# Performance work log

Hardware: AMD Instinct MI355X
Metric: run time of the kernel (lower is better)

Reference implementation:

```python
import jax, jax.numpy as jnp
import numpy as np

DIM = 512
HEADS = 8
BLOCK = 64
EXPAND = 4
EPS = 1e-5


def _layernorm(x, g, b):
    m = jnp.mean(x, axis=-1, keepdims=True)
    v = jnp.mean((x - m) ** 2, axis=-1, keepdims=True)
    return (x - m) * jax.lax.rsqrt(v + EPS) * g + b


def setup_inputs() -> dict:
    key = jax.random.key(0)
    ks = jax.random.split(key, 8)
    B, L = 8, 4096
    x = jax.random.normal(ks[0], (B, DIM, L), dtype=jnp.float32)
    s = 0.02
    params = {
        'w_qkv': jax.random.normal(ks[1], (DIM, 3 * DIM), jnp.float32) * s,
        'b_qkv': jnp.zeros((3 * DIM,), jnp.float32),
        'w_proj': jax.random.normal(ks[2], (DIM, DIM), jnp.float32) * s,
        'b_proj': jnp.zeros((DIM,), jnp.float32),
        'ln1_g': jnp.ones((DIM,), jnp.float32),
        'ln1_b': jnp.zeros((DIM,), jnp.float32),
        'ln2_g': jnp.ones((DIM,), jnp.float32),
        'ln2_b': jnp.zeros((DIM,), jnp.float32),
        'w_ffn1': jax.random.normal(ks[3], (DIM, DIM * EXPAND), jnp.float32) * s,
        'b_ffn1': jnp.zeros((DIM * EXPAND,), jnp.float32),
        'w_ffn2': jax.random.normal(ks[4], (DIM * EXPAND // 2, DIM), jnp.float32) * s,
        'b_ffn2': jnp.zeros((DIM,), jnp.float32),
        'attn_scale': jnp.ones((DIM,), jnp.float32),
        'attn_bias': jnp.zeros((DIM,), jnp.float32),
        'mlp_scale': jnp.ones((DIM,), jnp.float32),
        'mlp_bias': jnp.zeros((DIM,), jnp.float32),
    }
    return {'x': x, **params}


def _block_attn(x, w_qkv, b_qkv, w_proj, b_proj):
    # x: (B, L, D); L % BLOCK == 0 (no padding branch)
    B, L, D = x.shape
    d = D // HEADS
    scale = d ** -0.5
    qkv = x @ w_qkv + b_qkv                       # (B, L, 3D)
    qkv = qkv.reshape(B, L, HEADS, 3 * d)         # per-head [q|k|v] layout (matches torch split)
    q, k, v = jnp.split(qkv, 3, axis=-1)          # each (B, L, H, d)
    nb = L // BLOCK
    def to_blocks(t):
        return t.transpose(0, 2, 1, 3).reshape(B, HEADS, nb, BLOCK, d)
    q, k, v = to_blocks(q), to_blocks(k), to_blocks(v)
    attn = jnp.einsum('bhnqd,bhnkd->bhnqk', q, k) * scale
    attn = jax.nn.softmax(attn, axis=-1)
    o = jnp.einsum('bhnqk,bhnkd->bhnqd', attn, v)  # (B,H,nb,BLOCK,d)
    o = o.reshape(B, HEADS, L, d).transpose(0, 2, 1, 3).reshape(B, L, D)
    return o @ w_proj + b_proj


def _glu_mlp(x, w1, b1, w2, b2):
    h = x @ w1 + b1
    out, gate = jnp.split(h, 2, axis=-1)
    h = out * jax.nn.silu(gate)
    return h @ w2 + b2


def reference(x, w_qkv, b_qkv, w_proj, b_proj, ln1_g, ln1_b, ln2_g, ln2_b,
              w_ffn1, b_ffn1, w_ffn2, b_ffn2, attn_scale, attn_bias,
              mlp_scale, mlp_bias):
    # x: (B, DIM, L) channel-first, transposed inside like the torch module
    xt = x.transpose(0, 2, 1)                      # (B, L, D)
    # post-norm (prenorm=False)
    a = _block_attn(xt, w_qkv, b_qkv, w_proj, b_proj)
    a = a * attn_scale + attn_bias
    h = _layernorm(a + xt, ln1_g, ln1_b)
    m = _glu_mlp(h, w_ffn1, b_ffn1, w_ffn2, b_ffn2)
    m = m * mlp_scale + mlp_bias
    out = _layernorm(m + h, ln2_g, ln2_b)
    return out.transpose(0, 2, 1)                  # back to (B, DIM, L)
```

## Files before the change

### kernel.cpp

```cpp
#include <hip/hip_runtime.h>

#define DIM   512
#define LSEQ  4096
#define BATCH 8
#define NTOK  (BATCH * LSEQ)
#define NCHUNK 4
#define MCH   (NTOK / NCHUNK)
#define FCH   (NTOK / 2)

typedef __bf16 bf16_t;
typedef bf16_t bf16x8 __attribute__((ext_vector_type(8)));
typedef float  f32x4  __attribute__((ext_vector_type(4)));

__device__ __forceinline__ unsigned short f2bf(float f) {
  unsigned u = __builtin_bit_cast(unsigned, f);
  unsigned r = u + 0x7fffu + ((u >> 16) & 1u);
  return (unsigned short)(r >> 16);
}
__device__ __forceinline__ float bf2f(unsigned short s) {
  return __builtin_bit_cast(float, ((unsigned)s) << 16);
}
__device__ __forceinline__ bf16x8 ld_frag(const unsigned short* p) {
  uint4 v = *reinterpret_cast<const uint4*>(p);
  return __builtin_bit_cast(bf16x8, v);
}
__device__ __forceinline__ void gload16(const unsigned short* g, unsigned short* l) {
  __builtin_amdgcn_global_load_lds(
      (const __attribute__((address_space(1))) unsigned int*)(const void*)g,
      (__attribute__((address_space(3))) unsigned int*)(void*)l, 16, 0, 0);
}

__global__ __launch_bounds__(256) void prep_w(
    const float* __restrict__ W, unsigned short* __restrict__ out,
    int N, int NB, int ffn1) {
  const int idx = blockIdx.x * 256 + threadIdx.x;
  const int j0 = (idx & 7) * 8;
  const int nn = (idx >> 3) & 127;
  const int nbkt = idx >> 10;
  const int nb = nbkt % NB;
  const int kt = nbkt / NB;
  int wcol;
  if (ffn1) {
    int isg = (nn >> 5) & 1;
    int gcol = ((nn >> 6) << 5) + (((nn >> 4) & 1) << 4) + (nn & 15);
    wcol = isg * 1024 + nb * 64 + gcol;
  } else {
    wcol = nb * 128 + nn;
  }
  const int s = (nn & 7) << 3;
  union { unsigned short us[8]; uint4 u; } r;
#pragma unroll
  for (int t = 0; t < 8; ++t) {
    int row = kt * 64 + ((j0 ^ s) + t);
    r.us[t] = f2bf(W[(size_t)row * N + wcol]);
  }
  *reinterpret_cast<uint4*>(out + (size_t)nbkt * 8192 + nn * 64 + j0) = r.u;
}

__global__ __launch_bounds__(256) void transpose_in(
    const float* __restrict__ in, unsigned short* __restrict__ out) {
  __shared__ float tile[64][65];
  const int b = blockIdx.z;
  const int r0 = blockIdx.y * 64, c0 = blockIdx.x * 64;
  const float* ip = in + ((size_t)b * 512 + r0) * 4096 + c0;
#pragma unroll
  for (int i = 0; i < 16; ++i) {
    int flat = i * 256 + threadIdx.x;
    int r = flat >> 6, c = flat & 63;
    tile[r][c] = ip[(size_t)r * 4096 + c];
  }
  __syncthreads();
#pragma unroll
  for (int i = 0; i < 16; ++i) {
    int flat = i * 256 + threadIdx.x;
    int r = flat >> 6, c = flat & 63;
    out[((size_t)b * 4096 + c0 + r) * 512 + r0 + c] = f2bf(tile[c][r]);
  }
}

template <bool SCALERES>
__global__ __launch_bounds__(256, 2) void gemm_kernel(
    const unsigned short* __restrict__ A, const unsigned short* __restrict__ Wt,
    const float* __restrict__ bias, const float* __restrict__ scale,
    const float* __restrict__ bias2, const unsigned short* __restrict__ res,
    unsigned short* __restrict__ Cout, int N, int K, int nxb) {
  __shared__ unsigned short As[128 * 64];
  __shared__ unsigned short Bs[256 * 64];
  const int tid = threadIdx.x, lane = tid & 63, wave = tid >> 6;
  const int l15 = lane & 15, hi8 = (lane >> 4) * 8;
  const int wm = wave >> 1, wn = wave & 1;
  const int cpx = gridDim.x >> 3;
  const int sid = (blockIdx.x & 7) * cpx + (blockIdx.x >> 3);
  const int by = sid / nxb, bx = sid - by * nxb;
  const int row0 = by * 128, col0 = bx * 256;

  const unsigned short* abase =
      A + (size_t)(row0 + (lane >> 3)) * K + 8 * ((lane & 7) ^ (lane >> 3));
  const unsigned short* bbase = Wt + (size_t)(2 * bx) * 8192 + lane * 8;
  const size_t bstride = (size_t)(N >> 7) * 8192;

  f32x4 acc[4][8] = {};

  for (int kt = 0; kt < K; kt += 64) {
#pragma unroll
    for (int c = 0; c < 4; ++c) {
      const int ch = wave * 4 + c;
      gload16(abase + (size_t)(ch * 8) * K + kt, &As[ch * 512]);
    }
#pragma unroll
    for (int c = 0; c < 8; ++c) {
      const int cb = wave * 8 + c;
      gload16(bbase + (size_t)(kt >> 6) * bstride + cb * 512, &Bs[cb * 512]);
    }
    __syncthreads();
#pragma unroll
    for (int kk = 0; kk < 2; ++kk) {
      const int kbs = kk * 32 + hi8;
      bf16x8 af[4], bfr[8];
#pragma unroll
      for (int m = 0; m < 4; ++m) {
        int r = wm * 64 + m * 16 + l15;
        af[m] = ld_frag(&As[r * 64 + (kbs ^ ((r & 7) << 3))]);
      }
#pragma unroll
      for (int n = 0; n < 8; ++n) {
        int rb = wn * 128 + n * 16 + l15;
        bfr[n] = ld_frag(&Bs[rb * 64 + (kbs ^ ((rb & 7) << 3))]);
      }
#pragma unroll
      for (int m = 0; m < 4; ++m)
#pragma unroll
        for (int n = 0; n < 8; ++n)
          acc[m][n] = __builtin_amdgcn_mfma_f32_16x16x32_bf16(
              af[m], bfr[n], acc[m][n], 0, 0, 0);
    }
    __syncthreads();
  }
#pragma unroll
  for (int m = 0; m < 4; ++m) {
#pragma unroll
    for (int n = 0; n < 8; ++n) {
      const int col = col0 + wn * 128 + n * 16 + l15;
      const float b1 = bias[col];
      float sc = 1.f, b2 = 0.f;
      if constexpr (SCALERES) { sc = scale[col]; b2 = bias2[col]; }
#pragma unroll
      for (int r = 0; r < 4; ++r) {
        const int row = row0 + wm * 64 + m * 16 + (lane >> 4) * 4 + r;
        float v = acc[m][n][r] + b1;
        if constexpr (SCALERES) {
          v = v * sc + b2;
          v += bf2f(res[(size_t)row * N + col]);
        }
        Cout[(size_t)row * N + col] = f2bf(v);
      }
    }
  }
}

__global__ __launch_bounds__(256, 2) void ffn1glu_kernel(
    const unsigned short* __restrict__ A, const unsigned short* __restrict__ Wt,
    const float* __restrict__ b1, unsigned short* __restrict__ g, int nxb) {
  __shared__ unsigned short As[128 * 64];
  __shared__ unsigned short Bs[256 * 64];
  const int tid = threadIdx.x, lane = tid & 63, wave = tid >> 6;
  const int l15 = lane & 15, hi8 = (lane >> 4) * 8;
  const int wm = wave >> 1, wn = wave & 1;
  const int cpx = gridDim.x >> 3;
  const int sid = (blockIdx.x & 7) * cpx + (blockIdx.x >> 3);
  const int by = sid / nxb, bx = sid - by * nxb;
  const int row0 = by * 128;
  const int K = 512;

  const unsigned short* abase =
      A + (size_t)(row0 + (lane >> 3)) * K + 8 * ((lane & 7) ^ (lane >> 3));
  const unsigned short* bbase = Wt + (size_t)(2 * bx) * 8192 + lane * 8;
  const size_t bstride = (size_t)16 * 8192;

  f32x4 acc[4][8] = {};

  for (int kt = 0; kt < K; kt += 64) {
#pragma unroll
    for (int c = 0; c < 4; ++c) {
      const int ch = wave * 4 + c;
      gload16(abase + (size_t)(ch * 8) * K + kt, &As[ch * 512]);
    }
#pragma unroll
    for (int c = 0; c < 8; ++c) {
      const int cb = wave * 8 + c;
      gload16(bbase + (size_t)(kt >> 6) * bstride + cb * 512, &Bs[cb * 512]);
    }
    __syncthreads();
#pragma unroll
    for (int kk = 0; kk < 2; ++kk) {
      const int kbs = kk * 32 + hi8;
      bf16x8 af[4], bfr[8];
#pragma unroll
      for (int m = 0; m < 4; ++m) {
        int r = wm * 64 + m * 16 + l15;
        af[m] = ld_frag(&As[r * 64 + (kbs ^ ((r & 7) << 3))]);
      }
#pragma unroll
      for (int n = 0; n < 8; ++n) {
        int rb = wn * 128 + n * 16 + l15;
        bfr[n] = ld_frag(&Bs[rb * 64 + (kbs ^ ((rb & 7) << 3))]);
      }
#pragma unroll
      for (int m = 0; m < 4; ++m)
#pragma unroll
        for (int n = 0; n < 8; ++n)
          acc[m][n] = __builtin_amdgcn_mfma_f32_16x16x32_bf16(
              af[m], bfr[n], acc[m][n], 0, 0, 0);
    }
    __syncthreads();
  }
#pragma unroll
  for (int m = 0; m < 4; ++m) {
#pragma unroll
    for (int np = 0; np < 4; ++np) {
      const int n = (np & 1) + (np >> 1) * 4;
      const int sub = ((n & 4) ? 32 : 0) + (n & 1) * 16 + l15;
      const int gc = (2 * bx + wn) * 64 + sub;
      const float bo = b1[gc];
      const float bg = b1[1024 + gc];
#pragma unroll
      for (int r = 0; r < 4; ++r) {
        const int row = row0 + wm * 64 + m * 16 + (lane >> 4) * 4 + r;
        float o  = acc[m][n][r] + bo;
        float ga = acc[m][n + 2][r] + bg;
        float s  = ga / (1.f + __expf(-ga));
        g[(size_t)row * 1024 + gc] = f2bf(o * s);
      }
    }
  }
}

__global__ __launch_bounds__(256) void attn_kernel(
    const unsigned short* __restrict__ qkv, unsigned short* __restrict__ out) {
  __shared__ unsigned short Qs[64 * 64];
  __shared__ unsigned short Ks[64 * 64];
  __shared__ unsigned short Vs[64 * 64];
  __shared__ unsigned short Ps[64 * 64];
  const int id = blockIdx.x;
  const int h = id & 7, blk = id >> 3;
  const size_t tok0 = (size_t)blk * 64;
  const unsigned short* base = qkv + tok0 * 1536 + h * 192;
  const int tid = threadIdx.x, lane = tid & 63, wave = tid >> 6;

#pragma unroll
  for (int i = 0; i < 2; ++i) {
    int flat = i * 2048 + tid * 8;
    int r = flat >> 6, c = flat & 63;
    const unsigned short* p = base + (size_t)r * 1536 + c;
    uint4 q8 = *reinterpret_cast<const uint4*>(p);
    uint4 k8 = *reinterpret_cast<const uint4*>(p + 64);
    uint4 v8 = *reinterpret_cast<const uint4*>(p + 128);
    int us = r * 64 + (c ^ ((r & 7) << 3));
    *reinterpret_cast<uint4*>(&Qs[us]) = q8;
    *reinterpret_cast<uint4*>(&Ks[us]) = k8;
    const unsigned short* ve = reinterpret_cast<const unsigned short*>(&v8);
#pragma unroll
    for (int j = 0; j < 8; ++j) {
      int d = c + j;
      Vs[d * 64 + (r ^ ((d & 7) << 3))] = ve[j];
    }
  }
  __syncthreads();

  f32x4 sacc[4] = {};
#pragma unroll
  for (int kk = 0; kk < 64; kk += 32) {
    const int kb = kk + (lane >> 4) * 8;
    const int rq = wave * 16 + (lane & 15);
    bf16x8 aq = ld_frag(&Qs[rq * 64 + (kb ^ ((rq & 7) << 3))]);
#pragma unroll
    for (int n = 0; n < 4; ++n) {
      const int rk = n * 16 + (lane & 15);
      bf16x8 bk = ld_frag(&Ks[rk * 64 + (kb ^ ((rk & 7) << 3))]);
      sacc[n] = __builtin_amdgcn_mfma_f32_16x16x32_bf16(aq, bk, sacc[n], 0, 0, 0);
    }
  }
#pragma unroll
  for (int r = 0; r < 4; ++r) {
    float mx = -1e30f;
#pragma unroll
    for (int n = 0; n < 4; ++n) mx = fmaxf(mx, sacc[n][r]);
#pragma unroll
    for (int msk = 1; msk < 16; msk <<= 1) mx = fmaxf(mx, __shfl_xor(mx, msk));
    float sum = 0.f;
#pragma unroll
    for (int n = 0; n < 4; ++n) {
      float e = __expf((sacc[n][r] - mx) * 0.125f);
      sacc[n][r] = e;
      sum += e;
    }
#pragma unroll
    for (int msk = 1; msk < 16; msk <<= 1) sum += __shfl_xor(sum, msk);
    const float inv = 1.f / sum;
    const int row = wave * 16 + (lane >> 4) * 4 + r;
#pragma unroll
    for (int n = 0; n < 4; ++n) {
      int col = n * 16 + (lane & 15);
      Ps[row * 64 + (col ^ ((row & 7) << 3))] = f2bf(sacc[n][r] * inv);
    }
  }
  __syncthreads();

  f32x4 oacc[4] = {};
#pragma unroll
  for (int kk = 0; kk < 64; kk += 32) {
    const int kb = kk + (lane >> 4) * 8;
    const int rp = wave * 16 + (lane & 15);
    bf16x8 ap = ld_frag(&Ps[rp * 64 + (kb ^ ((rp & 7) << 3))]);
#pragma unroll
    for (int n = 0; n < 4; ++n) {
      const int rv = n * 16 + (lane & 15);
      bf16x8 bv = ld_frag(&Vs[rv * 64 + (kb ^ ((rv & 7) << 3))]);
      oacc[n] = __builtin_amdgcn_mfma_f32_16x16x32_bf16(ap, bv, oacc[n], 0, 0, 0);
    }
  }
#pragma unroll
  for (int n = 0; n < 4; ++n) {
    const int col = n * 16 + (lane & 15);
#pragma unroll
    for (int r = 0; r < 4; ++r) {
      const int row = wave * 16 + (lane >> 4) * 4 + r;
      out[(tok0 + row) * 512 + h * 64 + col] = f2bf(oacc[n][r]);
    }
  }
}

__global__ __launch_bounds__(256) void ln_kernel(
    const unsigned short* __restrict__ in, const float* __restrict__ gam,
    const float* __restrict__ bet, unsigned short* __restrict__ out) {
  const int wave = threadIdx.x >> 6, lane = threadIdx.x & 63;
  const size_t tok = (size_t)blockIdx.x * 4 + wave;
  const unsigned short* p = in + tok * DIM + lane * 8;
  uint4 raw = *reinterpret_cast<const uint4*>(p);
  const unsigned short* us = reinterpret_cast<const unsigned short*>(&raw);
  float x[8];
#pragma unroll
  for (int j = 0; j < 8; ++j) x[j] = bf2f(us[j]);
  float s = 0.f;
#pragma unroll
  for (int j = 0; j < 8; ++j) s += x[j];
#pragma unroll
  for (int m = 1; m < 64; m <<= 1) s += __shfl_xor(s, m);
  const float mean = s * (1.f / 512.f);
  float vr = 0.f;
#pragma unroll
  for (int j = 0; j < 8; ++j) { x[j] -= mean; vr += x[j] * x[j]; }
#pragma unroll
  for (int m = 1; m < 64; m <<= 1) vr += __shfl_xor(vr, m);
  const float rs = rsqrtf(vr * (1.f / 512.f) + 1e-5f);
  alignas(16) float gv[8], bv[8];
  *reinterpret_cast<float4*>(&gv[0]) = *reinterpret_cast<const float4*>(gam + lane * 8);
  *reinterpret_cast<float4*>(&gv[4]) = *reinterpret_cast<const float4*>(gam + lane * 8 + 4);
  *reinterpret_cast<float4*>(&bv[0]) = *reinterpret_cast<const float4*>(bet + lane * 8);
  *reinterpret_cast<float4*>(&bv[4]) = *reinterpret_cast<const float4*>(bet + lane * 8 + 4);
  union { unsigned short us[8]; uint4 u; } rr;
#pragma unroll
  for (int j = 0; j < 8; ++j) rr.us[j] = f2bf(x[j] * rs * gv[j] + bv[j]);
  unsigned short* q = out + tok * DIM + lane * 8;
  *reinterpret_cast<uint4*>(q) = rr.u;
}

__global__ __launch_bounds__(256) void ln_stats(
    const unsigned short* __restrict__ in, float2* __restrict__ stats) {
  const int wave = threadIdx.x >> 6, lane = threadIdx.x & 63;
  const size_t tok = (size_t)blockIdx.x * 4 + wave;
  const unsigned short* p = in + tok * DIM + lane * 8;
  uint4 raw = *reinterpret_cast<const uint4*>(p);
  const unsigned short* us = reinterpret_cast<const unsigned short*>(&raw);
  float x[8], s = 0.f;
#pragma unroll
  for (int j = 0; j < 8; ++j) { x[j] = bf2f(us[j]); s += x[j]; }
#pragma unroll
  for (int m = 1; m < 64; m <<= 1) s += __shfl_xor(s, m);
  const float mean = s * (1.f / 512.f);
  float vr = 0.f;
#pragma unroll
  for (int j = 0; j < 8; ++j) { float d = x[j] - mean; vr += d * d; }
#pragma unroll
  for (int m = 1; m < 64; m <<= 1) vr += __shfl_xor(vr, m);
  if (lane == 0) stats[tok] = make_float2(mean, rsqrtf(vr * (1.f / 512.f) + 1e-5f));
}

__global__ __launch_bounds__(256) void transpose_norm(
    const unsigned short* __restrict__ in, const float2* __restrict__ stats,
    const float* __restrict__ gam, const float* __restrict__ bet,
    float* __restrict__ out, int batch0) {
  __shared__ float tile[64][65];
  const int bz = blockIdx.z;
  const int b = batch0 + bz;
  const int t0 = blockIdx.y * 64, d0 = blockIdx.x * 64;
#pragma unroll
  for (int i = 0; i < 2; ++i) {
    int flat = i * 256 + threadIdx.x;
    int r = flat >> 3, cg = flat & 7;
    const size_t tokL = (size_t)bz * 4096 + t0 + r;
    uint4 raw = *reinterpret_cast<const uint4*>(in + tokL * 512 + d0 + cg * 8);
    const unsigned short* us = reinterpret_cast<const unsigned short*>(&raw);
    const float2 st = stats[tokL];
    alignas(16) float gv[8], bv[8];
    *reinterpret_cast<float4*>(&gv[0]) = *reinterpret_cast<const float4*>(gam + d0 + cg * 8);
    *reinterpret_cast<float4*>(&gv[4]) = *reinterpret_cast<const float4*>(gam + d0 + cg * 8 + 4);
    *reinterpret_cast<float4*>(&bv[0]) = *reinterpret_cast<const float4*>(bet + d0 + cg * 8);
    *reinterpret_cast<float4*>(&bv[4]) = *reinterpret_cast<const float4*>(bet + d0 + cg * 8 + 4);
#pragma unroll
    for (int j = 0; j < 8; ++j)
      tile[r][cg * 8 + j] = (bf2f(us[j]) - st.x) * st.y * gv[j] + bv[j];
  }
  __syncthreads();
#pragma unroll
  for (int i = 0; i < 16; ++i) {
    int flat = i * 256 + threadIdx.x;
    int r = flat >> 6, c = flat & 63;
    out[((size_t)b * 512 + d0 + r) * 4096 + t0 + c] = tile[c][r];
  }
}

extern "C" void kernel_launch(void* const* d_in, const int* in_sizes, int n_in,
                              void* d_out, int out_size, void* d_ws, size_t ws_size,
                              hipStream_t stream) {
  const float* x          = (const float*)d_in[0];
  const float* w_qkv      = (const float*)d_in[1];
  const float* b_qkv      = (const float*)d_in[2];
  const float* w_proj     = (const float*)d_in[3];
  const float* b_proj     = (const float*)d_in[4];
  const float* ln1_g      = (const float*)d_in[5];
  const float* ln1_b      = (const float*)d_in[6];
  const float* ln2_g      = (const float*)d_in[7];
  const float* ln2_b      = (const float*)d_in[8];
  const float* w_ffn1     = (const float*)d_in[9];
  const float* b_ffn1     = (const float*)d_in[10];
  const float* w_ffn2     = (const float*)d_in[11];
  const float* b_ffn2     = (const float*)d_in[12];
  const float* attn_scale = (const float*)d_in[13];
  const float* attn_bias  = (const float*)d_in[14];
  const float* mlp_scale  = (const float*)d_in[15];
  const float* mlp_bias   = (const float*)d_in[16];

  char* ws = (char*)d_ws;
  const size_t MiB = 1024ull * 1024ull;
  unsigned short* wqkvT  = (unsigned short*)(ws + 0);
  unsigned short* wprojT = (unsigned short*)(ws + 3 * MiB / 2);
  unsigned short* wffn1T = (unsigned short*)(ws + 2 * MiB);
  unsigned short* wffn2T = (unsigned short*)(ws + 4 * MiB);
  unsigned short* xt     = (unsigned short*)(ws + 5 * MiB);
  unsigned short* qkvH   = (unsigned short*)(ws + 37 * MiB);
  unsigned short* gbufC  = (unsigned short*)(ws + 5 * MiB);
  unsigned short* mresC  = (unsigned short*)(ws + 37 * MiB);
  float2*         st2    = (float2*)(ws + 53 * MiB);
  unsigned short* ares  = (unsigned short*)d_out;
  unsigned short* attnO = (unsigned short*)d_out + (size_t)NTOK * 512;
  unsigned short* hbuf  = (unsigned short*)d_out + (size_t)NTOK * 512;

  dim3 B256(256);
  prep_w<<<dim3(384), B256, 0, stream>>>(w_qkv,  wqkvT,  1536, 12, 0);
  prep_w<<<dim3(128), B256, 0, stream>>>(w_proj, wprojT,  512,  4, 0);
  prep_w<<<dim3(512), B256, 0, stream>>>(w_ffn1, wffn1T, 2048, 16, 1);
  prep_w<<<dim3(256), B256, 0, stream>>>(w_ffn2, wffn2T,  512,  4, 0);
  transpose_in<<<dim3(64, 8, 8), B256, 0, stream>>>(x, xt);
  for (int c = 0; c < NCHUNK; ++c) {
    gemm_kernel<false><<<dim3(6 * (MCH / 128)), B256, 0, stream>>>(
        xt + (size_t)c * MCH * 512, wqkvT, b_qkv, nullptr, nullptr, nullptr,
        qkvH, 1536, 512, 6);
    attn_kernel<<<dim3(MCH / 64 * 8), B256, 0, stream>>>(
        qkvH, attnO + (size_t)c * MCH * 512);
  }
  gemm_kernel<true><<<dim3(2 * (NTOK / 128)), B256, 0, stream>>>(
      attnO, wprojT, b_proj, attn_scale, attn_bias, xt, ares, 512, 512, 2);
  ln_kernel<<<dim3(NTOK / 4), B256, 0, stream>>>(ares, ln1_g, ln1_b, hbuf);
  for (int c = 0; c < 2; ++c) {
    const unsigned short* hC = hbuf + (size_t)c * FCH * 512;
    ffn1glu_kernel<<<dim3(8 * (FCH / 128)), B256, 0, stream>>>(
        hC, wffn1T, b_ffn1, gbufC, 8);
    gemm_kernel<true><<<dim3(2 * (FCH / 128)), B256, 0, stream>>>(
        gbufC, wffn2T, b_ffn2, mlp_scale, mlp_bias, hC, mresC, 512, 1024, 2);
    ln_stats<<<dim3(FCH / 4), B256, 0, stream>>>(mresC, st2);
    transpose_norm<<<dim3(8, 64, 4), B256, 0, stream>>>(
        mresC, st2, ln2_g, ln2_b, (float*)d_out, c * 4);
  }
}
```

Baseline: 368.9 us.

## Fuse output projection with LayerNorm1 and enlarge FFN1 GLU tiles

```diff
diff --git a/kernel.cpp b/kernel.cpp
--- a/kernel.cpp
+++ b/kernel.cpp
@@ -158,10 +158,119 @@
   }
 }
 
-__global__ __launch_bounds__(256, 2) void ffn1glu_kernel(
+__global__ __launch_bounds__(512, 2) void proj_ln_kernel(
+    const unsigned short* __restrict__ A, const unsigned short* __restrict__ Wt,
+    const float* __restrict__ bias, const float* __restrict__ scale,
+    const float* __restrict__ bias2, const unsigned short* __restrict__ res,
+    const float* __restrict__ gam, const float* __restrict__ bet,
+    unsigned short* __restrict__ H) {
+  __shared__ unsigned short As[128 * 64];
+  __shared__ unsigned short Bs[512 * 64];
+  const int tid = threadIdx.x, lane = tid & 63, wave = tid >> 6;
+  const int l15 = lane & 15, hi8 = (lane >> 4) * 8;
+  const int wm = wave >> 2, wn = wave & 3;
+  const int cpx = gridDim.x >> 3;
+  const int by = (blockIdx.x & 7) * cpx + (blockIdx.x >> 3);
+  const int row0 = by * 128;
+  const int K = 512, NB = 4;
+
+  const unsigned short* abase =
+      A + (size_t)(row0 + (lane >> 3)) * K + 8 * ((lane & 7) ^ (lane >> 3));
+
+  f32x4 acc[4][8] = {};
+
+  for (int kt6 = 0; kt6 < K / 64; ++kt6) {
+#pragma unroll
+    for (int c = 0; c < 2; ++c) {
+      const int ch = c * 8 + wave;
+      gload16(abase + (size_t)(ch * 8) * K + kt6 * 64, &As[ch * 512]);
+    }
+#pragma unroll
+    for (int c = 0; c < 8; ++c) {
+      const int cb = c * 8 + wave;
+      gload16(Wt + ((size_t)kt6 * NB + (cb >> 4)) * 8192 + (cb & 15) * 512 + lane * 8,
+              &Bs[cb * 512]);
+    }
+    __syncthreads();
+#pragma unroll
+    for (int kk = 0; kk < 2; ++kk) {
+      const int kbs = kk * 32 + hi8;
+      bf16x8 af[4], bfr[8];
+#pragma unroll
+      for (int m = 0; m < 4; ++m) {
+        int r = wm * 64 + m * 16 + l15;
+        af[m] = ld_frag(&As[r * 64 + (kbs ^ ((r & 7) << 3))]);
+      }
+#pragma unroll
+      for (int n = 0; n < 8; ++n) {
+        int cn = wn * 128 + n * 16 + l15;
+        bfr[n] = ld_frag(&Bs[cn * 64 + (kbs ^ ((cn & 7) << 3))]);
+      }
+#pragma unroll
+      for (int m = 0; m < 4; ++m)
+#pragma unroll
+        for (int n = 0; n < 8; ++n)
+          acc[m][n] = __builtin_amdgcn_mfma_f32_16x16x32_bf16(
+              af[m], bfr[n], acc[m][n], 0, 0, 0);
+    }
+    __syncthreads();
+  }
+
+  float bb[8], sc[8], b2[8], gv[8], bv[8];
+#pragma unroll
+  for (int n = 0; n < 8; ++n) {
+    const int col = wn * 128 + n * 16 + l15;
+    bb[n] = bias[col]; sc[n] = scale[col]; b2[n] = bias2[col];
+    gv[n] = gam[col];  bv[n] = bet[col];
+  }
+  float2* part = (float2*)As;
+#pragma unroll
+  for (int m = 0; m < 4; ++m)
+#pragma unroll
+    for (int r = 0; r < 4; ++r) {
+      const int brow = wm * 64 + m * 16 + (lane >> 4) * 4 + r;
+      const size_t rbase = (size_t)(row0 + brow) * 512;
+      float s = 0.f, q = 0.f;
+#pragma unroll
+      for (int n = 0; n < 8; ++n) {
+        const int col = wn * 128 + n * 16 + l15;
+        float v = (acc[m][n][r] + bb[n]) * sc[n] + b2[n] + bf2f(res[rbase + col]);
+        acc[m][n][r] = v;
+        s += v; q += v * v;
+      }
+#pragma unroll
+      for (int msk = 1; msk < 16; msk <<= 1) {
+        s += __shfl_xor(s, msk);
+        q += __shfl_xor(q, msk);
+      }
+      if (l15 == 0) part[brow * 4 + wn] = make_float2(s, q);
+    }
+  __syncthreads();
+#pragma unroll
+  for (int m = 0; m < 4; ++m)
+#pragma unroll
+    for (int r = 0; r < 4; ++r) {
+      const int brow = wm * 64 + m * 16 + (lane >> 4) * 4 + r;
+      float2 p0 = part[brow * 4 + 0], p1 = part[brow * 4 + 1];
+      float2 p2 = part[brow * 4 + 2], p3 = part[brow * 4 + 3];
+      const float S = p0.x + p1.x + p2.x + p3.x;
+      const float Q = p0.y + p1.y + p2.y + p3.y;
+      const float mean = S * (1.f / 512.f);
+      const float var = Q * (1.f / 512.f) - mean * mean;
+      const float rstd = rsqrtf(var + 1e-5f);
+      const size_t rbase = (size_t)(row0 + brow) * 512;
+#pragma unroll
+      for (int n = 0; n < 8; ++n) {
+        const int col = wn * 128 + n * 16 + l15;
+        H[rbase + col] = f2bf((acc[m][n][r] - mean) * rstd * gv[n] + bv[n]);
+      }
+    }
+}
+
+__global__ __launch_bounds__(512, 2) void ffn1glu_kernel(
     const unsigned short* __restrict__ A, const unsigned short* __restrict__ Wt,
     const float* __restrict__ b1, unsigned short* __restrict__ g, int nxb) {
-  __shared__ unsigned short As[128 * 64];
+  __shared__ unsigned short As[256 * 64];
   __shared__ unsigned short Bs[256 * 64];
   const int tid = threadIdx.x, lane = tid & 63, wave = tid >> 6;
   const int l15 = lane & 15, hi8 = (lane >> 4) * 8;
@@ -169,26 +278,25 @@
   const int cpx = gridDim.x >> 3;
   const int sid = (blockIdx.x & 7) * cpx + (blockIdx.x >> 3);
   const int by = sid / nxb, bx = sid - by * nxb;
-  const int row0 = by * 128;
-  const int K = 512;
+  const int row0 = by * 256;
+  const int K = 512, NB = 16;
 
   const unsigned short* abase =
       A + (size_t)(row0 + (lane >> 3)) * K + 8 * ((lane & 7) ^ (lane >> 3));
-  const unsigned short* bbase = Wt + (size_t)(2 * bx) * 8192 + lane * 8;
-  const size_t bstride = (size_t)16 * 8192;
 
   f32x4 acc[4][8] = {};
 
-  for (int kt = 0; kt < K; kt += 64) {
+  for (int kt6 = 0; kt6 < K / 64; ++kt6) {
 #pragma unroll
     for (int c = 0; c < 4; ++c) {
-      const int ch = wave * 4 + c;
-      gload16(abase + (size_t)(ch * 8) * K + kt, &As[ch * 512]);
-    }
-#pragma unroll
-    for (int c = 0; c < 8; ++c) {
-      const int cb = wave * 8 + c;
-      gload16(bbase + (size_t)(kt >> 6) * bstride + cb * 512, &Bs[cb * 512]);
+      const int ch = c * 8 + wave;
+      gload16(abase + (size_t)(ch * 8) * K + kt6 * 64, &As[ch * 512]);
+    }
+#pragma unroll
+    for (int c = 0; c < 4; ++c) {
+      const int cb = c * 8 + wave;
+      gload16(Wt + ((size_t)kt6 * NB + 2 * bx + (cb >> 4)) * 8192 + (cb & 15) * 512 + lane * 8,
+              &Bs[cb * 512]);
     }
     __syncthreads();
 #pragma unroll
@@ -202,8 +310,8 @@
       }
 #pragma unroll
       for (int n = 0; n < 8; ++n) {
-        int rb = wn * 128 + n * 16 + l15;
-        bfr[n] = ld_frag(&Bs[rb * 64 + (kbs ^ ((rb & 7) << 3))]);
+        int cn = wn * 128 + n * 16 + l15;
+        bfr[n] = ld_frag(&Bs[cn * 64 + (kbs ^ ((cn & 7) << 3))]);
       }
 #pragma unroll
       for (int m = 0; m < 4; ++m)
@@ -328,41 +436,6 @@
       out[(tok0 + row) * 512 + h * 64 + col] = f2bf(oacc[n][r]);
     }
   }
-}
-
-__global__ __launch_bounds__(256) void ln_kernel(
-    const unsigned short* __restrict__ in, const float* __restrict__ gam,
-    const float* __restrict__ bet, unsigned short* __restrict__ out) {
-  const int wave = threadIdx.x >> 6, lane = threadIdx.x & 63;
-  const size_t tok = (size_t)blockIdx.x * 4 + wave;
-  const unsigned short* p = in + tok * DIM + lane * 8;
-  uint4 raw = *reinterpret_cast<const uint4*>(p);
-  const unsigned short* us = reinterpret_cast<const unsigned short*>(&raw);
-  float x[8];
-#pragma unroll
-  for (int j = 0; j < 8; ++j) x[j] = bf2f(us[j]);
-  float s = 0.f;
-#pragma unroll
-  for (int j = 0; j < 8; ++j) s += x[j];
-#pragma unroll
-  for (int m = 1; m < 64; m <<= 1) s += __shfl_xor(s, m);
-  const float mean = s * (1.f / 512.f);
-  float vr = 0.f;
-#pragma unroll
-  for (int j = 0; j < 8; ++j) { x[j] -= mean; vr += x[j] * x[j]; }
-#pragma unroll
-  for (int m = 1; m < 64; m <<= 1) vr += __shfl_xor(vr, m);
-  const float rs = rsqrtf(vr * (1.f / 512.f) + 1e-5f);
-  alignas(16) float gv[8], bv[8];
-  *reinterpret_cast<float4*>(&gv[0]) = *reinterpret_cast<const float4*>(gam + lane * 8);
-  *reinterpret_cast<float4*>(&gv[4]) = *reinterpret_cast<const float4*>(gam + lane * 8 + 4);
-  *reinterpret_cast<float4*>(&bv[0]) = *reinterpret_cast<const float4*>(bet + lane * 8);
-  *reinterpret_cast<float4*>(&bv[4]) = *reinterpret_cast<const float4*>(bet + lane * 8 + 4);
-  union { unsigned short us[8]; uint4 u; } rr;
-#pragma unroll
-  for (int j = 0; j < 8; ++j) rr.us[j] = f2bf(x[j] * rs * gv[j] + bv[j]);
-  unsigned short* q = out + tok * DIM + lane * 8;
-  *reinterpret_cast<uint4*>(q) = rr.u;
 }
 
 __global__ __launch_bounds__(256) void ln_stats(
@@ -452,11 +525,10 @@
   unsigned short* gbufC  = (unsigned short*)(ws + 5 * MiB);
   unsigned short* mresC  = (unsigned short*)(ws + 37 * MiB);
   float2*         st2    = (float2*)(ws + 53 * MiB);
-  unsigned short* ares  = (unsigned short*)d_out;
   unsigned short* attnO = (unsigned short*)d_out + (size_t)NTOK * 512;
   unsigned short* hbuf  = (unsigned short*)d_out + (size_t)NTOK * 512;
 
-  dim3 B256(256);
+  dim3 B256(256), B512(512);
   prep_w<<<dim3(384), B256, 0, stream>>>(w_qkv,  wqkvT,  1536, 12, 0);
   prep_w<<<dim3(128), B256, 0, stream>>>(w_proj, wprojT,  512,  4, 0);
   prep_w<<<dim3(512), B256, 0, stream>>>(w_ffn1, wffn1T, 2048, 16, 1);
@@ -469,12 +541,11 @@
     attn_kernel<<<dim3(MCH / 64 * 8), B256, 0, stream>>>(
         qkvH, attnO + (size_t)c * MCH * 512);
   }
-  gemm_kernel<true><<<dim3(2 * (NTOK / 128)), B256, 0, stream>>>(
-      attnO, wprojT, b_proj, attn_scale, attn_bias, xt, ares, 512, 512, 2);
-  ln_kernel<<<dim3(NTOK / 4), B256, 0, stream>>>(ares, ln1_g, ln1_b, hbuf);
+  proj_ln_kernel<<<dim3(NTOK / 128), B512, 0, stream>>>(
+      attnO, wprojT, b_proj, attn_scale, attn_bias, xt, ln1_g, ln1_b, hbuf);
   for (int c = 0; c < 2; ++c) {
     const unsigned short* hC = hbuf + (size_t)c * FCH * 512;
-    ffn1glu_kernel<<<dim3(8 * (FCH / 128)), B256, 0, stream>>>(
+    ffn1glu_kernel<<<dim3(8 * (FCH / 256)), B512, 0, stream>>>(
         hC, wffn1T, b_ffn1, gbufC, 8);
     gemm_kernel<true><<<dim3(2 * (FCH / 128)), B256, 0, stream>>>(
         gbufC, wffn2T, b_ffn2, mlp_scale, mlp_bias, hC, mresC, 512, 1024, 2);
```

New measurement: 376.8 us. +2.1%, slower.

## Enlarge GEMM tiles to 256x256 with 512-thread blocks

Applied to the files above, without the earlier changes.

```diff
diff --git a/kernel.cpp b/kernel.cpp
--- a/kernel.cpp
+++ b/kernel.cpp
@@ -79,12 +79,12 @@
 }
 
 template <bool SCALERES>
-__global__ __launch_bounds__(256, 2) void gemm_kernel(
+__global__ __launch_bounds__(512, 2) void gemm256(
     const unsigned short* __restrict__ A, const unsigned short* __restrict__ Wt,
     const float* __restrict__ bias, const float* __restrict__ scale,
     const float* __restrict__ bias2, const unsigned short* __restrict__ res,
     unsigned short* __restrict__ Cout, int N, int K, int nxb) {
-  __shared__ unsigned short As[128 * 64];
+  __shared__ unsigned short As[256 * 64];
   __shared__ unsigned short Bs[256 * 64];
   const int tid = threadIdx.x, lane = tid & 63, wave = tid >> 6;
   const int l15 = lane & 15, hi8 = (lane >> 4) * 8;
@@ -92,25 +92,25 @@
   const int cpx = gridDim.x >> 3;
   const int sid = (blockIdx.x & 7) * cpx + (blockIdx.x >> 3);
   const int by = sid / nxb, bx = sid - by * nxb;
-  const int row0 = by * 128, col0 = bx * 256;
+  const int row0 = by * 256, col0 = bx * 256;
+  const int NB = N >> 7;
 
   const unsigned short* abase =
       A + (size_t)(row0 + (lane >> 3)) * K + 8 * ((lane & 7) ^ (lane >> 3));
-  const unsigned short* bbase = Wt + (size_t)(2 * bx) * 8192 + lane * 8;
-  const size_t bstride = (size_t)(N >> 7) * 8192;
 
   f32x4 acc[4][8] = {};
 
-  for (int kt = 0; kt < K; kt += 64) {
+  for (int kt6 = 0; kt6 < (K >> 6); ++kt6) {
 #pragma unroll
     for (int c = 0; c < 4; ++c) {
-      const int ch = wave * 4 + c;
-      gload16(abase + (size_t)(ch * 8) * K + kt, &As[ch * 512]);
-    }
-#pragma unroll
-    for (int c = 0; c < 8; ++c) {
-      const int cb = wave * 8 + c;
-      gload16(bbase + (size_t)(kt >> 6) * bstride + cb * 512, &Bs[cb * 512]);
+      const int ch = c * 8 + wave;
+      gload16(abase + (size_t)(ch * 8) * K + kt6 * 64, &As[ch * 512]);
+    }
+#pragma unroll
+    for (int c = 0; c < 4; ++c) {
+      const int cb = c * 8 + wave;
+      gload16(Wt + ((size_t)kt6 * NB + 2 * bx + (cb >> 4)) * 8192 + (cb & 15) * 512 + lane * 8,
+              &Bs[cb * 512]);
     }
     __syncthreads();
 #pragma unroll
@@ -124,8 +124,8 @@
       }
 #pragma unroll
       for (int n = 0; n < 8; ++n) {
-        int rb = wn * 128 + n * 16 + l15;
-        bfr[n] = ld_frag(&Bs[rb * 64 + (kbs ^ ((rb & 7) << 3))]);
+        int cn = wn * 128 + n * 16 + l15;
+        bfr[n] = ld_frag(&Bs[cn * 64 + (kbs ^ ((cn & 7) << 3))]);
       }
 #pragma unroll
       for (int m = 0; m < 4; ++m)
@@ -158,10 +158,10 @@
   }
 }
 
-__global__ __launch_bounds__(256, 2) void ffn1glu_kernel(
+__global__ __launch_bounds__(512, 2) void ffn1glu_kernel(
     const unsigned short* __restrict__ A, const unsigned short* __restrict__ Wt,
     const float* __restrict__ b1, unsigned short* __restrict__ g, int nxb) {
-  __shared__ unsigned short As[128 * 64];
+  __shared__ unsigned short As[256 * 64];
   __shared__ unsigned short Bs[256 * 64];
   const int tid = threadIdx.x, lane = tid & 63, wave = tid >> 6;
   const int l15 = lane & 15, hi8 = (lane >> 4) * 8;
@@ -169,26 +169,25 @@
   const int cpx = gridDim.x >> 3;
   const int sid = (blockIdx.x & 7) * cpx + (blockIdx.x >> 3);
   const int by = sid / nxb, bx = sid - by * nxb;
-  const int row0 = by * 128;
-  const int K = 512;
+  const int row0 = by * 256;
+  const int K = 512, NB = 16;
 
   const unsigned short* abase =
       A + (size_t)(row0 + (lane >> 3)) * K + 8 * ((lane & 7) ^ (lane >> 3));
-  const unsigned short* bbase = Wt + (size_t)(2 * bx) * 8192 + lane * 8;
-  const size_t bstride = (size_t)16 * 8192;
 
   f32x4 acc[4][8] = {};
 
-  for (int kt = 0; kt < K; kt += 64) {
+  for (int kt6 = 0; kt6 < K / 64; ++kt6) {
 #pragma unroll
     for (int c = 0; c < 4; ++c) {
-      const int ch = wave * 4 + c;
-      gload16(abase + (size_t)(ch * 8) * K + kt, &As[ch * 512]);
-    }
-#pragma unroll
-    for (int c = 0; c < 8; ++c) {
-      const int cb = wave * 8 + c;
-      gload16(bbase + (size_t)(kt >> 6) * bstride + cb * 512, &Bs[cb * 512]);
+      const int ch = c * 8 + wave;
+      gload16(abase + (size_t)(ch * 8) * K + kt6 * 64, &As[ch * 512]);
+    }
+#pragma unroll
+    for (int c = 0; c < 4; ++c) {
+      const int cb = c * 8 + wave;
+      gload16(Wt + ((size_t)kt6 * NB + 2 * bx + (cb >> 4)) * 8192 + (cb & 15) * 512 + lane * 8,
+              &Bs[cb * 512]);
     }
     __syncthreads();
 #pragma unroll
@@ -202,8 +201,8 @@
       }
 #pragma unroll
       for (int n = 0; n < 8; ++n) {
-        int rb = wn * 128 + n * 16 + l15;
-        bfr[n] = ld_frag(&Bs[rb * 64 + (kbs ^ ((rb & 7) << 3))]);
+        int cn = wn * 128 + n * 16 + l15;
+        bfr[n] = ld_frag(&Bs[cn * 64 + (kbs ^ ((cn & 7) << 3))]);
       }
 #pragma unroll
       for (int m = 0; m < 4; ++m)
@@ -456,27 +455,27 @@
   unsigned short* attnO = (unsigned short*)d_out + (size_t)NTOK * 512;
   unsigned short* hbuf  = (unsigned short*)d_out + (size_t)NTOK * 512;
 
-  dim3 B256(256);
+  dim3 B256(256), B512(512);
   prep_w<<<dim3(384), B256, 0, stream>>>(w_qkv,  wqkvT,  1536, 12, 0);
   prep_w<<<dim3(128), B256, 0, stream>>>(w_proj, wprojT,  512,  4, 0);
   prep_w<<<dim3(512), B256, 0, stream>>>(w_ffn1, wffn1T, 2048, 16, 1);
   prep_w<<<dim3(256), B256, 0, stream>>>(w_ffn2, wffn2T,  512,  4, 0);
   transpose_in<<<dim3(64, 8, 8), B256, 0, stream>>>(x, xt);
   for (int c = 0; c < NCHUNK; ++c) {
-    gemm_kernel<false><<<dim3(6 * (MCH / 128)), B256, 0, stream>>>(
+    gemm256<false><<<dim3(6 * (MCH / 256)), B512, 0, stream>>>(
         xt + (size_t)c * MCH * 512, wqkvT, b_qkv, nullptr, nullptr, nullptr,
         qkvH, 1536, 512, 6);
     attn_kernel<<<dim3(MCH / 64 * 8), B256, 0, stream>>>(
         qkvH, attnO + (size_t)c * MCH * 512);
   }
-  gemm_kernel<true><<<dim3(2 * (NTOK / 128)), B256, 0, stream>>>(
+  gemm256<true><<<dim3(2 * (NTOK / 256)), B512, 0, stream>>>(
       attnO, wprojT, b_proj, attn_scale, attn_bias, xt, ares, 512, 512, 2);
   ln_kernel<<<dim3(NTOK / 4), B256, 0, stream>>>(ares, ln1_g, ln1_b, hbuf);
   for (int c = 0; c < 2; ++c) {
     const unsigned short* hC = hbuf + (size_t)c * FCH * 512;
-    ffn1glu_kernel<<<dim3(8 * (FCH / 128)), B256, 0, stream>>>(
+    ffn1glu_kernel<<<dim3(8 * (FCH / 256)), B512, 0, stream>>>(
         hC, wffn1T, b_ffn1, gbufC, 8);
-    gemm_kernel<true><<<dim3(2 * (FCH / 128)), B256, 0, stream>>>(
+    gemm256<true><<<dim3(2 * (FCH / 256)), B512, 0, stream>>>(
         gbufC, wffn2T, b_ffn2, mlp_scale, mlp_bias, hC, mresC, 512, 1024, 2);
     ln_stats<<<dim3(FCH / 4), B256, 0, stream>>>(mresC, st2);
     transpose_norm<<<dim3(8, 64, 4), B256, 0, stream>>>(
```

After: 405.7 us. +10.0%, slower.
